# Kernel optimization log

Measured on AMD Instinct MI355X. Metric: run time of the kernel, lower is better.

The kernel has to match this reference:

```python
import jax, jax.numpy as jnp
import numpy as np
from jax import lax

EPS = 1e-12  # torch F.normalize eps


def _l2norm(x):
    n = jnp.linalg.norm(x, axis=-1, keepdims=True)
    return x / jnp.maximum(n, EPS)


def _conv1x1(x, w):
    # x: [B,C,H,W], w: [O,C] (1x1 conv, no bias)
    return jnp.einsum('bchw,oc->bohw', x, w)


def _se(x, w1, w2):
    # AdaptiveAvgPool2d(1) -> 1x1 conv (no bias) -> ReLU -> 1x1 conv (no bias) -> ReLU
    p = jnp.mean(x, axis=(2, 3))                      # [B,256]
    h = jax.nn.relu(jnp.einsum('bc,oc->bo', p, w1))   # [B,320]
    return jax.nn.relu(jnp.einsum('bc,oc->bo', h, w2))  # [B,1280]


def _tdec(x, wk_w, wk_b, wv_w, wv_b, red_w, rise_w, rise_b):
    # fc_reduce: 1x1 conv 256->128
    x1 = _conv1x1(x, red_w)                           # [B,128,H,W]
    B, d, H, W = x1.shape
    t = x1.reshape(B, d, H * W).transpose(0, 2, 1)    # [B,N,128] tokens
    # same WK linear produces both q and k (xq == xk in the source)
    k = _l2norm(jnp.einsum('bnd,ed->bne', t, wk_w) + wk_b)  # [B,N,128]
    v = _l2norm(jnp.einsum('bnd,ed->bne', t, wv_w) + wv_b)  # [B,N,128]
    # bmm(wq[B,d,N], wk[B,N,d]) -> [B,d,d] channel gram, temp 30 softmax
    attn = jax.nn.softmax(jnp.einsum('bni,bnj->bij', k, k) * 30.0, axis=-1)
    # bmm(attn[B,d,d], v^T[B,d,N]) -> [B,d,N], reshape back to map
    ot = jnp.einsum('bij,bnj->bin', attn, v).reshape(B, d, H, W)
    return _conv1x1(ot, rise_w) + rise_b[None, :, None, None]


def _fwd(x0, x1, x2, x3, x4, spec_w1, spec_w2, comm_w1, comm_w2,
         pre_w, pre_b, wk1_w, wk1_b, wv1_w, wv1_b, red1_w, rise1_w, rise1_b,
         wk2_w, wk2_b, wv2_w, wv2_b, red2_w, rise2_w, rise2_b):
    xs = jnp.stack([x0, x1, x2, x3, x4])              # [5,B,256,H,W]
    B = x0.shape[0]
    # reduce(lambda x,y: abs(x-y), down_x)
    diff = x0
    for xi in (x1, x2, x3, x4):
        diff = jnp.abs(diff - xi)
    ssum = xs.sum(axis=0)
    wd = jax.nn.softmax(_se(diff, spec_w1, spec_w2).reshape(B, 5, 256), axis=1)
    ws = jax.nn.softmax(_se(ssum, comm_w1, comm_w2).reshape(B, 5, 256), axis=1)
    # v2[i] = x_i*wd_i + x_i*ws_i + x_i ; v3 = sum_i v2[i]
    v3 = jnp.einsum('sbchw,bsc->bchw', xs, wd + ws + 1.0)
    pre = jax.nn.relu(
        lax.conv_general_dilated(v3, pre_w, (1, 1), ((1, 1), (1, 1)),
                                 dimension_numbers=('NCHW', 'OIHW', 'NCHW'))
        + pre_b[None, :, None, None])
    f1 = _tdec(pre, wk1_w, wk1_b, wv1_w, wv1_b, red1_w, rise1_w, rise1_b)
    f3 = _tdec(f1 + v3, wk2_w, wk2_b, wv2_w, wv2_b, red2_w, rise2_w, rise2_b)
    return f1 + f3 + v3


def setup_inputs() -> dict:
    key = jax.random.key(0)
    ks = iter(jax.random.split(key, 40))
    B, C, H, W = 16, 256, 64, 64

    def p(shape, scale=0.05):
        return jax.random.normal(next(ks), shape, jnp.float32) * scale

    inp = {f'x{i}': jax.random.normal(next(ks), (B, C, H, W), jnp.float32) for i in range(5)}
    inp.update(
        spec_w1=p((320, 256)), spec_w2=p((1280, 320)),
        comm_w1=p((320, 256)), comm_w2=p((1280, 320)),
        pre_w=p((256, 256, 3, 3)), pre_b=p((256,)),
        wk1_w=p((128, 128)), wk1_b=p((128,)), wv1_w=p((128, 128)), wv1_b=p((128,)),
        red1_w=p((128, 256)), rise1_w=p((256, 128)), rise1_b=p((256,)),
        wk2_w=p((128, 128)), wk2_b=p((128,)), wv2_w=p((128, 128)), wv2_b=p((128,)),
        red2_w=p((128, 256)), rise2_w=p((256, 128)), rise2_b=p((256,)),
    )
    return inp


def reference(x0, x1, x2, x3, x4, spec_w1, spec_w2, comm_w1, comm_w2,
              pre_w, pre_b, wk1_w, wk1_b, wv1_w, wv1_b, red1_w, rise1_w, rise1_b,
              wk2_w, wk2_b, wv2_w, wv2_b, red2_w, rise2_w, rise2_b):
    return _fwd(x0, x1, x2, x3, x4, spec_w1, spec_w2, comm_w1, comm_w2,
                pre_w, pre_b, wk1_w, wk1_b, wv1_w, wv1_b, red1_w, rise1_w, rise1_b,
                wk2_w, wk2_b, wv2_w, wv2_b, red2_w, rise2_w, rise2_b)
```

## Files before the change

kernel.cpp:

```cpp
#include <hip/hip_runtime.h>

#define DI __device__ __forceinline__

typedef short s16x8 __attribute__((ext_vector_type(8)));
typedef unsigned short u16;
typedef u16 u16x4 __attribute__((ext_vector_type(4)));
typedef u16 u16x8 __attribute__((ext_vector_type(8)));
typedef u16 u16x16 __attribute__((ext_vector_type(16)));
typedef float f32x4 __attribute__((ext_vector_type(4)));
typedef _Float16 f16;
typedef f16 f16x4 __attribute__((ext_vector_type(4)));

DI float bf2f(u16 v) { return __builtin_bit_cast(float, (unsigned)v << 16); }
DI u16 f2bf(float f) {
  unsigned u = __builtin_bit_cast(unsigned, f);
  return (u16)((u + 0x7fffu + ((u >> 16) & 1u)) >> 16);
}

__global__ void k_cast8(u16* __restrict__ dst,
    const float* __restrict__ s0, const float* __restrict__ s1,
    const float* __restrict__ s2, const float* __restrict__ s3,
    const float* __restrict__ s4, const float* __restrict__ s5,
    const float* __restrict__ s6, const float* __restrict__ s7) {
  int i = blockIdx.x * 256 + threadIdx.x;
  const float* src; int base;
  if (i < 32768) { src = s0; base = 0; }
  else if (i < 49152) { src = s1; base = 32768; }
  else if (i < 65536) { src = s2; base = 49152; }
  else if (i < 98304) { src = s3; base = 65536; }
  else if (i < 131072) { src = s4; base = 98304; }
  else if (i < 147456) { src = s5; base = 131072; }
  else if (i < 163840) { src = s6; base = 147456; }
  else { src = s7; base = 163840; }
  dst[i] = f2bf(src[i - base]);
}

__global__ void k_wconv(u16* __restrict__ dst, const float* __restrict__ src) {
  int i = blockIdx.x * 256 + threadIdx.x;
  if (i < 9 * 256 * 256) {
    int tap = i >> 16, rem = i & 65535;
    dst[i] = f2bf(src[(size_t)rem * 9 + tap]);
  }
}

__global__ __launch_bounds__(256) void k_pool(
    const float* __restrict__ x0, const float* __restrict__ x1,
    const float* __restrict__ x2, const float* __restrict__ x3,
    const float* __restrict__ x4, float* __restrict__ pd, float* __restrict__ ps,
    f16* __restrict__ hx1, f16* __restrict__ hx2,
    f16* __restrict__ hx3, f16* __restrict__ hx4) {
  int c = blockIdx.x, b = blockIdx.y;
  size_t ebase = ((size_t)b * 256 + c) * 4096 + threadIdx.x * 4;
  float sd = 0.f, sm = 0.f;
#pragma unroll
  for (int it = 0; it < 4; ++it) {
    size_t off = ebase + it * 1024;
    f32x4 a0 = *(const f32x4*)(x0 + off);
    f32x4 a1 = *(const f32x4*)(x1 + off);
    f32x4 a2 = *(const f32x4*)(x2 + off);
    f32x4 a3 = *(const f32x4*)(x3 + off);
    f32x4 a4 = *(const f32x4*)(x4 + off);
    f16x4 h1, h2, h3, h4;
#pragma unroll
    for (int e = 0; e < 4; ++e) {
      float d = fabsf(a0[e] - a1[e]); d = fabsf(d - a2[e]); d = fabsf(d - a3[e]); d = fabsf(d - a4[e]);
      sd += d; sm += a0[e] + a1[e] + a2[e] + a3[e] + a4[e];
      h1[e] = (f16)a1[e]; h2[e] = (f16)a2[e]; h3[e] = (f16)a3[e]; h4[e] = (f16)a4[e];
    }
    *(f16x4*)(hx1 + off) = h1;
    *(f16x4*)(hx2 + off) = h2;
    *(f16x4*)(hx3 + off) = h3;
    *(f16x4*)(hx4 + off) = h4;
  }
  for (int o = 32; o; o >>= 1) { sd += __shfl_xor(sd, o); sm += __shfl_xor(sm, o); }
  __shared__ float rb[4][2];
  int wv = threadIdx.x >> 6, lane = threadIdx.x & 63;
  if (!lane) { rb[wv][0] = sd; rb[wv][1] = sm; }
  __syncthreads();
  if (!threadIdx.x) {
    float a = rb[0][0] + rb[1][0] + rb[2][0] + rb[3][0];
    float s2 = rb[0][1] + rb[1][1] + rb[2][1] + rb[3][1];
    pd[b * 256 + c] = a * (1.f / 4096.f);
    ps[b * 256 + c] = s2 * (1.f / 4096.f);
  }
}

__global__ __launch_bounds__(256) void k_se1(
    const float* __restrict__ pd, const float* __restrict__ ps,
    const float* __restrict__ sw1, const float* __restrict__ cw1,
    float* __restrict__ h1) {
  int b = blockIdx.y, z = blockIdx.z;
  int wv = threadIdx.x >> 6, lane = threadIdx.x & 63;
  int e = blockIdx.x * 4 + wv;
  const float* in = (z ? ps : pd) + b * 256;
  const float* w = (z ? cw1 : sw1) + (size_t)e * 256;
  float a = 0.f;
#pragma unroll
  for (int i = 0; i < 4; ++i) a += in[lane + 64 * i] * w[lane + 64 * i];
  for (int o = 32; o; o >>= 1) a += __shfl_xor(a, o);
  if (!lane) h1[((size_t)z * 16 + b) * 320 + e] = fmaxf(a, 0.f);
}

__global__ __launch_bounds__(256) void k_se2(
    const float* __restrict__ h1, const float* __restrict__ sw2,
    const float* __restrict__ cw2, float* __restrict__ h2) {
  int b = blockIdx.y, z = blockIdx.z;
  int wv = threadIdx.x >> 6, lane = threadIdx.x & 63;
  int e = blockIdx.x * 4 + wv;
  const float* in = h1 + ((size_t)z * 16 + b) * 320;
  const float* w = (z ? cw2 : sw2) + (size_t)e * 320;
  float a = 0.f;
#pragma unroll
  for (int i = 0; i < 5; ++i) a += in[lane + 64 * i] * w[lane + 64 * i];
  for (int o = 32; o; o >>= 1) a += __shfl_xor(a, o);
  if (!lane) h2[((size_t)z * 16 + b) * 1280 + e] = fmaxf(a, 0.f);
}

__global__ __launch_bounds__(256) void k_se3(
    const float* __restrict__ h2, float* __restrict__ wt) {
  int b = blockIdx.x, t = threadIdx.x;
  const float* Hs = h2 + (size_t)b * 1280;
  const float* Hc = h2 + (size_t)(16 + b) * 1280;
  float d0 = Hs[t], d1 = Hs[256 + t], d2 = Hs[512 + t], d3 = Hs[768 + t], d4 = Hs[1024 + t];
  float m = fmaxf(fmaxf(fmaxf(d0, d1), fmaxf(d2, d3)), d4);
  float e0 = expf(d0 - m), e1 = expf(d1 - m), e2 = expf(d2 - m), e3 = expf(d3 - m), e4 = expf(d4 - m);
  float inv = 1.f / (e0 + e1 + e2 + e3 + e4);
  float c0 = Hc[t], c1 = Hc[256 + t], c2 = Hc[512 + t], c3 = Hc[768 + t], c4 = Hc[1024 + t];
  float mc = fmaxf(fmaxf(fmaxf(c0, c1), fmaxf(c2, c3)), c4);
  float g0 = expf(c0 - mc), g1 = expf(c1 - mc), g2 = expf(c2 - mc), g3 = expf(c3 - mc), g4 = expf(c4 - mc);
  float ci = 1.f / (g0 + g1 + g2 + g3 + g4);
  size_t base = (size_t)b * 1280 + t;
  wt[base + 0 * 256] = e0 * inv + g0 * ci + 1.f;
  wt[base + 1 * 256] = e1 * inv + g1 * ci + 1.f;
  wt[base + 2 * 256] = e2 * inv + g2 * ci + 1.f;
  wt[base + 3 * 256] = e3 * inv + g3 * ci + 1.f;
  wt[base + 4 * 256] = e4 * inv + g4 * ci + 1.f;
}

__global__ __launch_bounds__(256) void k_v3(
    const float* __restrict__ x0, const f16* __restrict__ hx1,
    const f16* __restrict__ hx2, const f16* __restrict__ hx3,
    const f16* __restrict__ hx4, const float* __restrict__ wt,
    u16* __restrict__ v3b) {
  int h = blockIdx.x, b = blockIdx.y;
  __shared__ float W[1280];
  __shared__ u16 T[256][68];
  int t = threadIdx.x;
  for (int s = t; s < 1280; s += 256) W[s] = wt[(size_t)b * 1280 + s];
  __syncthreads();
  int csub = t >> 4, l16 = t & 15;
  size_t ebase = (size_t)b * 256 * 4096 + h * 64 + l16 * 4;
#pragma unroll 4
  for (int ci = 0; ci < 16; ++ci) {
    int c = ci * 16 + csub;
    size_t a = ebase + (size_t)c * 4096;
    f32x4 v0 = *(const f32x4*)(x0 + a);
    f16x4 v1 = *(const f16x4*)(hx1 + a);
    f16x4 v2 = *(const f16x4*)(hx2 + a);
    f16x4 v3 = *(const f16x4*)(hx3 + a);
    f16x4 v4 = *(const f16x4*)(hx4 + a);
    float w0 = W[c], w1 = W[256 + c], w2 = W[512 + c], w3 = W[768 + c], w4 = W[1024 + c];
    u16x4 ov;
#pragma unroll
    for (int e = 0; e < 4; ++e)
      ov[e] = f2bf(v0[e] * w0 + (float)v1[e] * w1 + (float)v2[e] * w2 +
                   (float)v3[e] * w3 + (float)v4[e] * w4);
    *(u16x4*)(&T[c][l16 * 4]) = ov;
  }
  __syncthreads();
  int w = t >> 2, oct = t & 3;
  size_t obase = ((size_t)b * 4096 + h * 64 + w) * 256;
  for (int pass = 0; pass < 8; ++pass) {
    int c0 = oct * 8 + pass * 32;
    u16x8 ov;
#pragma unroll
    for (int jj = 0; jj < 8; ++jj) ov[jj] = T[c0 + jj][w];
    *(u16x8*)(v3b + obase + c0) = ov;
  }
}

__global__ __launch_bounds__(256) void k_conv(
    const u16* __restrict__ v3b, const u16* __restrict__ Wt,
    const float* __restrict__ bias, u16* __restrict__ pre) {
  int o = blockIdx.x;
  int wg = (o & 7) * 128 + (o >> 3);
  int oh = wg & 1, hp = (wg >> 1) & 31, b = wg >> 6;
  __shared__ __align__(16) u16 Ain[4 * 64 * 40];
  __shared__ __align__(16) u16 Bls[2][128 * 40];
  int t = threadIdx.x, wv = t >> 6, lane = t & 63;
  int wm = (wv >> 1) * 64, wn = (wv & 1) * 64, fr = lane & 15, ko = lane >> 4;

  auto loadA = [&](int cc, int s) -> u16x16 {
    int r = s >> 7, rest = s & 127, w = rest >> 1, half = rest & 1;
    int hs = hp * 2 - 1 + r;
    u16x16 v = {};
    if ((unsigned)hs < 64u)
      v = *(const u16x16*)(v3b + (((size_t)b * 64 + hs) * 64 + w) * 256 + cc * 32 + half * 16);
    return v;
  };
  auto storeA = [&](int s, u16x16 v) {
    int r = s >> 7, rest = s & 127, w = rest >> 1, half = rest & 1;
    *(u16x16*)(Ain + (r * 64 + w) * 40 + half * 16) = v;
  };
  auto loadB = [&](int tap, int cc) -> u16x16 {
    int n = t >> 1, half = t & 1;
    return *(const u16x16*)(Wt + ((size_t)tap * 256 + oh * 128 + n) * 256 + cc * 32 + half * 16);
  };
  auto storeB = [&](int bsel, u16x16 v) {
    int n = t >> 1, half = t & 1;
    *(u16x16*)(Bls[bsel] + n * 40 + half * 16) = v;
  };

  u16x16 pA0 = loadA(0, t), pA1 = loadA(0, t + 256);
  u16x16 rB = loadB(0, 0);
  storeA(t, pA0); storeA(t + 256, pA1); storeB(0, rB);
  rB = loadB(1, 0);
  __syncthreads();

  f32x4 acc[4][4] = {};
  int buf = 0;
  for (int cc = 0; cc < 8; ++cc) {
#pragma unroll
    for (int tap = 0; tap < 9; ++tap) {
      const int dh = tap / 3 - 1, dw = tap % 3 - 1;
      s16x8 af[4], bfr[4];
#pragma unroll
      for (int i = 0; i < 4; ++i) {
        int m = wm + i * 16 + fr, r = m >> 6, wq = m & 63;
        int wqd = wq + dw;
        s16x8 v = {};
        if ((unsigned)wqd < 64u)
          v = *(const s16x8*)(Ain + ((r + dh + 1) * 64 + wqd) * 40 + ko * 8);
        af[i] = v;
      }
#pragma unroll
      for (int j = 0; j < 4; ++j)
        bfr[j] = *(const s16x8*)(Bls[buf] + (wn + j * 16 + fr) * 40 + ko * 8);
#pragma unroll
      for (int i = 0; i < 4; ++i)
#pragma unroll
        for (int j = 0; j < 4; ++j)
          acc[i][j] = __builtin_amdgcn_mfma_f32_16x16x32_bf16(af[i], bfr[j], acc[i][j], 0, 0, 0);
      const int u = cc * 9 + tap;
      if (u < 71) {
        if (tap == 8) {
          __syncthreads();
          storeA(t, pA0); storeA(t + 256, pA1);
        }
        storeB(buf ^ 1, rB);
        if (u + 2 <= 71) {
          const int un = u + 2;
          rB = loadB(un % 9, un / 9);
        }
        if (tap == 7 && cc < 7) { pA0 = loadA(cc + 1, t); pA1 = loadA(cc + 1, t + 256); }
        __syncthreads();
        buf ^= 1;
      }
    }
  }
#pragma unroll
  for (int i = 0; i < 4; ++i) {
    int m0 = wm + i * 16 + ko * 4;
#pragma unroll
    for (int j = 0; j < 4; ++j) {
      int och = oh * 128 + wn + j * 16 + fr;
      float bv = bias[och];
#pragma unroll
      for (int r = 0; r < 4; ++r) {
        float v = fmaxf(acc[i][j][r] + bv, 0.f);
        pre[((size_t)b * 4096 + hp * 128 + m0 + r) * 256 + och] = f2bf(v);
      }
    }
  }
}

__global__ __launch_bounds__(256) void k_qkv(
    const u16* __restrict__ in,
    const u16* __restrict__ redW,
    const u16* __restrict__ wkW,
    const u16* __restrict__ wvW,
    const float* __restrict__ kb, const float* __restrict__ vb,
    u16* __restrict__ vout,
    u16* __restrict__ khat) {
  int nt = blockIdx.x, b = blockIdx.y;
  const u16* Ab = in + ((size_t)b * 4096 + nt * 128) * 256;
  __shared__ __align__(16) u16 Ald[128 * 40];
  __shared__ __align__(16) u16 Bld[128 * 40];
  __shared__ __align__(16) u16 T[128 * 136];
  __shared__ float SS[2][128];
  int t = threadIdx.x, wv = t >> 6, lane = t & 63;
  int wm = (wv >> 1) * 64, wn = (wv & 1) * 64, fr = lane & 15, ko = lane >> 4;
  f32x4 acc[4][4] = {};
  for (int kc = 0; kc < 256; kc += 32) {
    for (int s = t; s < 512; s += 256) {
      int r = s >> 2, ks = s & 3;
      *(u16x8*)(Ald + r * 40 + ks * 8) = *(const u16x8*)(Ab + (size_t)r * 256 + kc + ks * 8);
    }
    for (int s = t; s < 512; s += 256) {
      int r = s >> 2, ks = s & 3;
      *(u16x8*)(Bld + r * 40 + ks * 8) = *(const u16x8*)(redW + (size_t)r * 256 + kc + ks * 8);
    }
    __syncthreads();
    s16x8 af[4], bf[4];
#pragma unroll
    for (int i = 0; i < 4; ++i) af[i] = *(const s16x8*)(Ald + (wm + i * 16 + fr) * 40 + ko * 8);
#pragma unroll
    for (int j = 0; j < 4; ++j) bf[j] = *(const s16x8*)(Bld + (wn + j * 16 + fr) * 40 + ko * 8);
#pragma unroll
    for (int i = 0; i < 4; ++i)
#pragma unroll
      for (int j = 0; j < 4; ++j)
        acc[i][j] = __builtin_amdgcn_mfma_f32_16x16x32_bf16(af[i], bf[j], acc[i][j], 0, 0, 0);
    __syncthreads();
  }
#pragma unroll
  for (int i = 0; i < 4; ++i)
#pragma unroll
    for (int j = 0; j < 4; ++j)
#pragma unroll
      for (int r = 0; r < 4; ++r)
        T[(wm + i * 16 + ko * 4 + r) * 136 + wn + j * 16 + fr] = f2bf(acc[i][j][r]);

  for (int z = 0; z < 2; ++z) {
    const u16* W = z ? wkW : wvW;
    const float* bias = z ? kb : vb;
    f32x4 a2[4][4] = {};
#pragma unroll
    for (int h = 0; h < 2; ++h) {
      __syncthreads();
      for (int s = t; s < 512; s += 256) {
        int r = s >> 2, ks = s & 3;
        *(u16x8*)(Ald + r * 40 + ks * 8) = *(const u16x8*)(W + (size_t)r * 128 + h * 64 + ks * 8);
      }
      for (int s = t; s < 512; s += 256) {
        int r = s >> 2, ks = s & 3;
        *(u16x8*)(Bld + r * 40 + ks * 8) = *(const u16x8*)(W + (size_t)r * 128 + h * 64 + 32 + ks * 8);
      }
      __syncthreads();
#pragma unroll
      for (int kk = 0; kk < 2; ++kk) {
        const u16* Bsrc = kk ? Bld : Ald;
        s16x8 af[4], bf[4];
#pragma unroll
        for (int i = 0; i < 4; ++i)
          af[i] = *(const s16x8*)(T + (size_t)(wm + i * 16 + fr) * 136 + h * 64 + kk * 32 + ko * 8);
#pragma unroll
        for (int j = 0; j < 4; ++j)
          bf[j] = *(const s16x8*)(Bsrc + (wn + j * 16 + fr) * 40 + ko * 8);
#pragma unroll
        for (int i = 0; i < 4; ++i)
#pragma unroll
          for (int j = 0; j < 4; ++j)
            a2[i][j] = __builtin_amdgcn_mfma_f32_16x16x32_bf16(af[i], bf[j], a2[i][j], 0, 0, 0);
      }
    }
    float bj[4];
#pragma unroll
    for (int j = 0; j < 4; ++j) bj[j] = bias[wn + j * 16 + fr];
    float pss[4][4];
#pragma unroll
    for (int i = 0; i < 4; ++i)
#pragma unroll
      for (int r = 0; r < 4; ++r) pss[i][r] = 0.f;
#pragma unroll
    for (int i = 0; i < 4; ++i)
#pragma unroll
      for (int j = 0; j < 4; ++j)
#pragma unroll
        for (int r = 0; r < 4; ++r) {
          float v = a2[i][j][r] + bj[j];
          a2[i][j][r] = v;
          pss[i][r] += v * v;
        }
#pragma unroll
    for (int m = 1; m < 16; m <<= 1)
#pragma unroll
      for (int i = 0; i < 4; ++i)
#pragma unroll
        for (int r = 0; r < 4; ++r) pss[i][r] += __shfl_xor(pss[i][r], m);
    if (fr == 0)
#pragma unroll
      for (int i = 0; i < 4; ++i)
#pragma unroll
        for (int r = 0; r < 4; ++r) SS[wv & 1][wm + i * 16 + ko * 4 + r] = pss[i][r];
    __syncthreads();
    float sc[4][4];
#pragma unroll
    for (int i = 0; i < 4; ++i)
#pragma unroll
      for (int r = 0; r < 4; ++r) {
        int tok = wm + i * 16 + ko * 4 + r;
        float s2 = SS[0][tok] + SS[1][tok];
        sc[i][r] = 1.f / fmaxf(sqrtf(s2), 1e-12f);
      }
#pragma unroll
    for (int i = 0; i < 4; ++i)
#pragma unroll
      for (int j = 0; j < 4; ++j)
#pragma unroll
        for (int r = 0; r < 4; ++r) a2[i][j][r] *= sc[i][r];
    if (z == 0) {
      size_t tokbase = (size_t)b * 4096 + nt * 128;
#pragma unroll
      for (int i = 0; i < 4; ++i)
#pragma unroll
        for (int j = 0; j < 4; ++j) {
          u16* dst = vout + (tokbase + wm + i * 16 + ko * 4) * 128 + wn + j * 16 + fr;
#pragma unroll
          for (int r = 0; r < 4; ++r) dst[(size_t)r * 128] = f2bf(a2[i][j][r]);
        }
    } else {
#pragma unroll
      for (int i = 0; i < 4; ++i)
#pragma unroll
        for (int j = 0; j < 4; ++j)
#pragma unroll
          for (int r = 0; r < 4; ++r)
            T[(size_t)(wn + j * 16 + fr) * 136 + wm + i * 16 + ko * 4 + r] = f2bf(a2[i][j][r]);
      __syncthreads();
      for (int s = t; s < 2048; s += 256) {
        int ch = s >> 4, sg = s & 15;
        *(u16x8*)(khat + ((size_t)b * 128 + ch) * 4096 + nt * 128 + sg * 8) =
            *(const u16x8*)(T + ch * 136 + sg * 8);
      }
    }
  }
}

template <int MODE>
__global__ __launch_bounds__(256) void k_pvrise(
    const u16* __restrict__ vbuf,
    const u16* __restrict__ attnb,
    const u16* __restrict__ riseW,
    const float* __restrict__ bias,
    const u16* __restrict__ add0, const u16* __restrict__ add1,
    u16* __restrict__ out0, u16* __restrict__ out1, float* __restrict__ outf) {
  int nt = blockIdx.x, b = blockIdx.y;
  const u16* Ab = vbuf + ((size_t)b * 4096 + nt * 128) * 128;
  const u16* Bb = attnb + (size_t)b * 128 * 128;
  __shared__ __align__(16) u16 Ald[128 * 40];
  __shared__ __align__(16) u16 Bld[128 * 40];
  __shared__ __align__(16) u16 T[128 * 136];
  int t = threadIdx.x, wv = t >> 6, lane = t & 63;
  int wm = (wv >> 1) * 64, wn = (wv & 1) * 64, fr = lane & 15, ko = lane >> 4;
  f32x4 acc[4][4] = {};
  for (int kc = 0; kc < 128; kc += 32) {
    for (int s = t; s < 512; s += 256) {
      int r = s >> 2, ks = s & 3;
      *(u16x8*)(Ald + r * 40 + ks * 8) = *(const u16x8*)(Ab + (size_t)r * 128 + kc + ks * 8);
    }
    for (int s = t; s < 512; s += 256) {
      int r = s >> 2, ks = s & 3;
      *(u16x8*)(Bld + r * 40 + ks * 8) = *(const u16x8*)(Bb + (size_t)r * 128 + kc + ks * 8);
    }
    __syncthreads();
    s16x8 af[4], bf[4];
#pragma unroll
    for (int i = 0; i < 4; ++i) af[i] = *(const s16x8*)(Ald + (wm + i * 16 + fr) * 40 + ko * 8);
#pragma unroll
    for (int j = 0; j < 4; ++j) bf[j] = *(const s16x8*)(Bld + (wn + j * 16 + fr) * 40 + ko * 8);
#pragma unroll
    for (int i = 0; i < 4; ++i)
#pragma unroll
      for (int j = 0; j < 4; ++j)
        acc[i][j] = __builtin_amdgcn_mfma_f32_16x16x32_bf16(af[i], bf[j], acc[i][j], 0, 0, 0);
    __syncthreads();
  }
#pragma unroll
  for (int i = 0; i < 4; ++i)
#pragma unroll
    for (int j = 0; j < 4; ++j)
#pragma unroll
      for (int r = 0; r < 4; ++r)
        T[(wm + i * 16 + ko * 4 + r) * 136 + wn + j * 16 + fr] = f2bf(acc[i][j][r]);

  size_t tokbase = (size_t)b * 4096 + nt * 128;
  for (int z = 0; z < 2; ++z) {
    const u16* W = riseW + (size_t)z * 128 * 128;
    f32x4 a2[4][4] = {};
#pragma unroll
    for (int h = 0; h < 2; ++h) {
      __syncthreads();
      for (int s = t; s < 512; s += 256) {
        int r = s >> 2, ks = s & 3;
        *(u16x8*)(Ald + r * 40 + ks * 8) = *(const u16x8*)(W + (size_t)r * 128 + h * 64 + ks * 8);
      }
      for (int s = t; s < 512; s += 256) {
        int r = s >> 2, ks = s & 3;
        *(u16x8*)(Bld + r * 40 + ks * 8) = *(const u16x8*)(W + (size_t)r * 128 + h * 64 + 32 + ks * 8);
      }
      __syncthreads();
#pragma unroll
      for (int kk = 0; kk < 2; ++kk) {
        const u16* Bsrc = kk ? Bld : Ald;
        s16x8 af[4], bf[4];
#pragma unroll
        for (int i = 0; i < 4; ++i)
          af[i] = *(const s16x8*)(T + (size_t)(wm + i * 16 + fr) * 136 + h * 64 + kk * 32 + ko * 8);
#pragma unroll
        for (int j = 0; j < 4; ++j)
          bf[j] = *(const s16x8*)(Bsrc + (wn + j * 16 + fr) * 40 + ko * 8);
#pragma unroll
        for (int i = 0; i < 4; ++i)
#pragma unroll
          for (int j = 0; j < 4; ++j)
            a2[i][j] = __builtin_amdgcn_mfma_f32_16x16x32_bf16(af[i], bf[j], a2[i][j], 0, 0, 0);
      }
    }
#pragma unroll
    for (int i = 0; i < 4; ++i) {
      int m0 = wm + i * 16 + ko * 4;
#pragma unroll
      for (int j = 0; j < 4; ++j) {
        int o = z * 128 + wn + j * 16 + fr;
        float bv = bias[o];
        size_t idx = (tokbase + m0) * 256 + o;
        if constexpr (MODE == 3) {
#pragma unroll
          for (int r = 0; r < 4; ++r) {
            float f1v = a2[i][j][r] + bv;
            out0[idx + (size_t)r * 256] = f2bf(f1v);
            out1[idx + (size_t)r * 256] = f2bf(f1v + bf2f(add0[idx + (size_t)r * 256]));
          }
        } else {
          f32x4 vv;
#pragma unroll
          for (int r = 0; r < 4; ++r)
            vv[r] = a2[i][j][r] + bv + bf2f(add0[idx + (size_t)r * 256]) +
                    bf2f(add1[idx + (size_t)r * 256]);
          *(f32x4*)(outf + ((size_t)b * 256 + o) * 4096 + nt * 128 + m0) = vv;
        }
      }
    }
  }
}

__global__ __launch_bounds__(256) void k_gram(const u16* __restrict__ kt, float* __restrict__ gp) {
  int ks = blockIdx.x, b = blockIdx.y;
  const u16* base = kt + (size_t)b * 128 * 4096 + ks * 256;
  __shared__ __align__(16) u16 Tld[128 * 40];
  int t = threadIdx.x, wv = t >> 6, lane = t & 63;
  int wm = (wv >> 1) * 64, wn = (wv & 1) * 64, fr = lane & 15, ko = lane >> 4;
  f32x4 acc[4][4] = {};
  for (int kc = 0; kc < 256; kc += 32) {
    for (int s = t; s < 512; s += 256) {
      int r = s >> 2, k2 = s & 3;
      *(u16x8*)(Tld + r * 40 + k2 * 8) = *(const u16x8*)(base + (size_t)r * 4096 + kc + k2 * 8);
    }
    __syncthreads();
    s16x8 af[4], bf[4];
#pragma unroll
    for (int i = 0; i < 4; ++i) af[i] = *(const s16x8*)(Tld + (wm + i * 16 + fr) * 40 + ko * 8);
#pragma unroll
    for (int j = 0; j < 4; ++j) bf[j] = *(const s16x8*)(Tld + (wn + j * 16 + fr) * 40 + ko * 8);
#pragma unroll
    for (int i = 0; i < 4; ++i)
#pragma unroll
      for (int j = 0; j < 4; ++j)
        acc[i][j] = __builtin_amdgcn_mfma_f32_16x16x32_bf16(af[i], bf[j], acc[i][j], 0, 0, 0);
    __syncthreads();
  }
  float* dst = gp + ((size_t)(ks * 16 + b) * 128) * 128;
#pragma unroll
  for (int i = 0; i < 4; ++i) {
    int m0 = wm + i * 16 + ko * 4;
#pragma unroll
    for (int j = 0; j < 4; ++j) {
      int nc = wn + j * 16 + fr;
#pragma unroll
      for (int r = 0; r < 4; ++r) dst[(size_t)(m0 + r) * 128 + nc] = acc[i][j][r];
    }
  }
}

__global__ void k_soft(const float* __restrict__ gp, u16* __restrict__ attn) {
  int i = blockIdx.x, b = blockIdx.y, l = threadIdx.x;
  float s0 = 0.f, s1 = 0.f;
  for (int ks = 0; ks < 16; ++ks) {
    const float* row = gp + (((size_t)ks * 16 + b) * 128 + i) * 128;
    s0 += row[l]; s1 += row[l + 64];
  }
  s0 *= 30.f; s1 *= 30.f;
  float m = fmaxf(s0, s1);
  for (int o = 32; o; o >>= 1) m = fmaxf(m, __shfl_xor(m, o));
  float e0 = expf(s0 - m), e1 = expf(s1 - m);
  float s = e0 + e1;
  for (int o = 32; o; o >>= 1) s += __shfl_xor(s, o);
  float inv = 1.f / s;
  u16* dst = attn + ((size_t)b * 128 + i) * 128;
  dst[l] = f2bf(e0 * inv);
  dst[l + 64] = f2bf(e1 * inv);
}

extern "C" void kernel_launch(void* const* d_in, const int* in_sizes, int n_in,
                              void* d_out, int out_size, void* d_ws, size_t ws_size,
                              hipStream_t stream) {
  (void)in_sizes; (void)n_in; (void)out_size; (void)ws_size;
  const float* x0 = (const float*)d_in[0];
  const float* x1 = (const float*)d_in[1];
  const float* x2 = (const float*)d_in[2];
  const float* x3 = (const float*)d_in[3];
  const float* x4 = (const float*)d_in[4];
  const float* spec_w1 = (const float*)d_in[5];
  const float* spec_w2 = (const float*)d_in[6];
  const float* comm_w1 = (const float*)d_in[7];
  const float* comm_w2 = (const float*)d_in[8];
  const float* pre_w = (const float*)d_in[9];
  const float* pre_bias = (const float*)d_in[10];
  const float* wk1_w = (const float*)d_in[11];
  const float* wk1_b = (const float*)d_in[12];
  const float* wv1_w = (const float*)d_in[13];
  const float* wv1_b = (const float*)d_in[14];
  const float* red1_w = (const float*)d_in[15];
  const float* rise1_w = (const float*)d_in[16];
  const float* rise1_b = (const float*)d_in[17];
  const float* wk2_w = (const float*)d_in[18];
  const float* wk2_b = (const float*)d_in[19];
  const float* wv2_w = (const float*)d_in[20];
  const float* wv2_b = (const float*)d_in[21];
  const float* red2_w = (const float*)d_in[22];
  const float* rise2_w = (const float*)d_in[23];
  const float* rise2_b = (const float*)d_in[24];
  float* out = (float*)d_out;

  char* wsp = (char*)d_ws;
  size_t off = 0;
  auto alloc = [&](size_t bytes) -> void* {
    off = (off + 255) & ~(size_t)255;
    void* p = wsp + off;
    off += bytes;
    return p;
  };
  float* pd = (float*)alloc(16 * 256 * 4);
  float* ps = (float*)alloc(16 * 256 * 4);
  float* h1b = (float*)alloc(2 * 16 * 320 * 4);
  float* h2b = (float*)alloc(2 * 16 * 1280 * 4);
  float* wtb = (float*)alloc(16 * 5 * 256 * 4);
  u16* v3b = (u16*)alloc((size_t)16 * 4096 * 256 * 2);
  u16* Wtc = (u16*)alloc((size_t)9 * 256 * 256 * 2);
  u16* wall = (u16*)alloc((size_t)196608 * 2);
  u16* red1b = wall;
  u16* wk1b = wall + 32768;
  u16* wv1b = wall + 49152;
  u16* rise1b = wall + 65536;
  u16* red2b = wall + 98304;
  u16* wk2b = wall + 131072;
  u16* wv2b = wall + 147456;
  u16* rise2b = wall + 163840;
  u16* pre = (u16*)alloc((size_t)16 * 4096 * 256 * 2);
  u16* tbuf = (u16*)alloc((size_t)16 * 4096 * 128 * 2);
  u16* khat = (u16*)alloc((size_t)16 * 4096 * 128 * 2);
  u16* vbuf = (u16*)alloc((size_t)16 * 4096 * 128 * 2);
  u16* attn = (u16*)alloc((size_t)16 * 128 * 128 * 2);
  u16* spacer = (u16*)alloc((size_t)16 * 4096 * 128 * 2);
  u16* f1b = (u16*)alloc((size_t)16 * 4096 * 256 * 2);
  (void)spacer;
  float* gpart = (float*)tbuf;
  u16* in2b = pre;
  f16* hx = (f16*)pre;
  const size_t HXN = (size_t)16 * 256 * 4096;
  f16* hx1 = hx;
  f16* hx2 = hx + HXN;
  f16* hx3 = hx + 2 * HXN;
  f16* hx4 = hx + 3 * HXN;

  k_cast8<<<dim3(768), 256, 0, stream>>>(wall, red1_w, wk1_w, wv1_w, rise1_w,
                                         red2_w, wk2_w, wv2_w, rise2_w);
  k_wconv<<<dim3(2304), 256, 0, stream>>>(Wtc, pre_w);

  k_pool<<<dim3(256, 16), 256, 0, stream>>>(x0, x1, x2, x3, x4, pd, ps, hx1, hx2, hx3, hx4);
  k_se1<<<dim3(80, 16, 2), 256, 0, stream>>>(pd, ps, spec_w1, comm_w1, h1b);
  k_se2<<<dim3(320, 16, 2), 256, 0, stream>>>(h1b, spec_w2, comm_w2, h2b);
  k_se3<<<dim3(16), 256, 0, stream>>>(h2b, wtb);
  k_v3<<<dim3(64, 16), 256, 0, stream>>>(x0, hx1, hx2, hx3, hx4, wtb, v3b);
  k_conv<<<dim3(1024), 256, 0, stream>>>(v3b, Wtc, pre_bias, pre);

  k_qkv<<<dim3(32, 16), 256, 0, stream>>>(pre, red1b, wk1b, wv1b, wk1_b, wv1_b, vbuf, khat);
  k_gram<<<dim3(16, 16), 256, 0, stream>>>(khat, gpart);
  k_soft<<<dim3(128, 16), 64, 0, stream>>>(gpart, attn);
  k_pvrise<3><<<dim3(32, 16), 256, 0, stream>>>(vbuf, attn, rise1b, rise1_b,
      v3b, nullptr, f1b, in2b, nullptr);

  k_qkv<<<dim3(32, 16), 256, 0, stream>>>(in2b, red2b, wk2b, wv2b, wk2_b, wv2_b, vbuf, khat);
  k_gram<<<dim3(16, 16), 256, 0, stream>>>(khat, gpart);
  k_soft<<<dim3(128, 16), 64, 0, stream>>>(gpart, attn);
  k_pvrise<4><<<dim3(32, 16), 256, 0, stream>>>(vbuf, attn, rise2b, rise2_b,
      f1b, v3b, nullptr, nullptr, out);
}
```

Before: 451.5 us.

## Fuse channel Gram computation into QKV kernel, drop separate gram pass

```diff
diff --git a/kernel.cpp b/kernel.cpp
--- a/kernel.cpp
+++ b/kernel.cpp
@@ -281,7 +281,7 @@
     const u16* __restrict__ wvW,
     const float* __restrict__ kb, const float* __restrict__ vb,
     u16* __restrict__ vout,
-    u16* __restrict__ khat) {
+    float* __restrict__ gp) {
   int nt = blockIdx.x, b = blockIdx.y;
   const u16* Ab = in + ((size_t)b * 4096 + nt * 128) * 256;
   __shared__ __align__(16) u16 Ald[128 * 40];
@@ -418,10 +418,31 @@
           for (int r = 0; r < 4; ++r)
             T[(size_t)(wn + j * 16 + fr) * 136 + wm + i * 16 + ko * 4 + r] = f2bf(a2[i][j][r]);
       __syncthreads();
-      for (int s = t; s < 2048; s += 256) {
-        int ch = s >> 4, sg = s & 15;
-        *(u16x8*)(khat + ((size_t)b * 128 + ch) * 4096 + nt * 128 + sg * 8) =
-            *(const u16x8*)(T + ch * 136 + sg * 8);
+      f32x4 g3[4][4] = {};
+      for (int kc = 0; kc < 128; kc += 32) {
+        s16x8 af[4], bf[4];
+#pragma unroll
+        for (int i = 0; i < 4; ++i)
+          af[i] = *(const s16x8*)(T + (size_t)(wm + i * 16 + fr) * 136 + kc + ko * 8);
+#pragma unroll
+        for (int j = 0; j < 4; ++j)
+          bf[j] = *(const s16x8*)(T + (size_t)(wn + j * 16 + fr) * 136 + kc + ko * 8);
+#pragma unroll
+        for (int i = 0; i < 4; ++i)
+#pragma unroll
+          for (int j = 0; j < 4; ++j)
+            g3[i][j] = __builtin_amdgcn_mfma_f32_16x16x32_bf16(af[i], bf[j], g3[i][j], 0, 0, 0);
+      }
+      float* dst = gp + ((size_t)(b * 32 + nt)) * 16384;
+#pragma unroll
+      for (int i = 0; i < 4; ++i) {
+        int m0 = wm + i * 16 + ko * 4;
+#pragma unroll
+        for (int j = 0; j < 4; ++j) {
+          int nc = wn + j * 16 + fr;
+#pragma unroll
+          for (int r = 0; r < 4; ++r) dst[(size_t)(m0 + r) * 128 + nc] = g3[i][j][r];
+        }
       }
     }
   }
@@ -535,49 +556,11 @@
   }
 }
 
-__global__ __launch_bounds__(256) void k_gram(const u16* __restrict__ kt, float* __restrict__ gp) {
-  int ks = blockIdx.x, b = blockIdx.y;
-  const u16* base = kt + (size_t)b * 128 * 4096 + ks * 256;
-  __shared__ __align__(16) u16 Tld[128 * 40];
-  int t = threadIdx.x, wv = t >> 6, lane = t & 63;
-  int wm = (wv >> 1) * 64, wn = (wv & 1) * 64, fr = lane & 15, ko = lane >> 4;
-  f32x4 acc[4][4] = {};
-  for (int kc = 0; kc < 256; kc += 32) {
-    for (int s = t; s < 512; s += 256) {
-      int r = s >> 2, k2 = s & 3;
-      *(u16x8*)(Tld + r * 40 + k2 * 8) = *(const u16x8*)(base + (size_t)r * 4096 + kc + k2 * 8);
-    }
-    __syncthreads();
-    s16x8 af[4], bf[4];
-#pragma unroll
-    for (int i = 0; i < 4; ++i) af[i] = *(const s16x8*)(Tld + (wm + i * 16 + fr) * 40 + ko * 8);
-#pragma unroll
-    for (int j = 0; j < 4; ++j) bf[j] = *(const s16x8*)(Tld + (wn + j * 16 + fr) * 40 + ko * 8);
-#pragma unroll
-    for (int i = 0; i < 4; ++i)
-#pragma unroll
-      for (int j = 0; j < 4; ++j)
-        acc[i][j] = __builtin_amdgcn_mfma_f32_16x16x32_bf16(af[i], bf[j], acc[i][j], 0, 0, 0);
-    __syncthreads();
-  }
-  float* dst = gp + ((size_t)(ks * 16 + b) * 128) * 128;
-#pragma unroll
-  for (int i = 0; i < 4; ++i) {
-    int m0 = wm + i * 16 + ko * 4;
-#pragma unroll
-    for (int j = 0; j < 4; ++j) {
-      int nc = wn + j * 16 + fr;
-#pragma unroll
-      for (int r = 0; r < 4; ++r) dst[(size_t)(m0 + r) * 128 + nc] = acc[i][j][r];
-    }
-  }
-}
-
 __global__ void k_soft(const float* __restrict__ gp, u16* __restrict__ attn) {
   int i = blockIdx.x, b = blockIdx.y, l = threadIdx.x;
   float s0 = 0.f, s1 = 0.f;
-  for (int ks = 0; ks < 16; ++ks) {
-    const float* row = gp + (((size_t)ks * 16 + b) * 128 + i) * 128;
+  for (int ks = 0; ks < 32; ++ks) {
+    const float* row = gp + ((size_t)(b * 32 + ks)) * 16384 + (size_t)i * 128;
     s0 += row[l]; s1 += row[l + 64];
   }
   s0 *= 30.f; s1 *= 30.f;
@@ -648,14 +631,12 @@
   u16* wv2b = wall + 147456;
   u16* rise2b = wall + 163840;
   u16* pre = (u16*)alloc((size_t)16 * 4096 * 256 * 2);
-  u16* tbuf = (u16*)alloc((size_t)16 * 4096 * 128 * 2);
-  u16* khat = (u16*)alloc((size_t)16 * 4096 * 128 * 2);
+  float* gpart = (float*)alloc((size_t)16 * 32 * 128 * 128 * 4);
   u16* vbuf = (u16*)alloc((size_t)16 * 4096 * 128 * 2);
   u16* attn = (u16*)alloc((size_t)16 * 128 * 128 * 2);
   u16* spacer = (u16*)alloc((size_t)16 * 4096 * 128 * 2);
   u16* f1b = (u16*)alloc((size_t)16 * 4096 * 256 * 2);
   (void)spacer;
-  float* gpart = (float*)tbuf;
   u16* in2b = pre;
   f16* hx = (f16*)pre;
   const size_t HXN = (size_t)16 * 256 * 4096;
@@ -675,14 +656,12 @@
   k_v3<<<dim3(64, 16), 256, 0, stream>>>(x0, hx1, hx2, hx3, hx4, wtb, v3b);
   k_conv<<<dim3(1024), 256, 0, stream>>>(v3b, Wtc, pre_bias, pre);
 
-  k_qkv<<<dim3(32, 16), 256, 0, stream>>>(pre, red1b, wk1b, wv1b, wk1_b, wv1_b, vbuf, khat);
-  k_gram<<<dim3(16, 16), 256, 0, stream>>>(khat, gpart);
+  k_qkv<<<dim3(32, 16), 256, 0, stream>>>(pre, red1b, wk1b, wv1b, wk1_b, wv1_b, vbuf, gpart);
   k_soft<<<dim3(128, 16), 64, 0, stream>>>(gpart, attn);
   k_pvrise<3><<<dim3(32, 16), 256, 0, stream>>>(vbuf, attn, rise1b, rise1_b,
       v3b, nullptr, f1b, in2b, nullptr);
 
-  k_qkv<<<dim3(32, 16), 256, 0, stream>>>(in2b, red2b, wk2b, wv2b, wk2_b, wv2_b, vbuf, khat);
-  k_gram<<<dim3(16, 16), 256, 0, stream>>>(khat, gpart);
+  k_qkv<<<dim3(32, 16), 256, 0, stream>>>(in2b, red2b, wk2b, wv2b, wk2_b, wv2_b, vbuf, gpart);
   k_soft<<<dim3(128, 16), 64, 0, stream>>>(gpart, attn);
   k_pvrise<4><<<dim3(32, 16), 256, 0, stream>>>(vbuf, attn, rise2b, rise2_b,
       f1b, v3b, nullptr, nullptr, out);
```

Result: faster. 437.4 us (-3.1%).
